# Kernel optimization log

Hardware: AMD Instinct MI355X
Metric: run time of the kernel (lower is better)

## Reference

```python
import jax, jax.numpy as jnp
import numpy as np

B, T_ENC, T_DEC = 64, 256, 200
MEL, R = 80, 2
ENC_DIM = 256   # must equal attention_context_dim (context = weighted sum of encoder outputs)
ATT = 256       # attention_rnn_units == attention_context_dim
DEC = 256       # decoder_rnn_units
PRE1, PRE2 = 256, 128


def _gru(x, h, wih, whh, bih, bhh):
    # torch.nn.GRUCell math; weights are (3*H, in) torch layout
    gi = x @ wih.T + bih
    gh = h @ whh.T + bhh
    i_r, i_z, i_n = jnp.split(gi, 3, axis=-1)
    h_r, h_z, h_n = jnp.split(gh, 3, axis=-1)
    r = jax.nn.sigmoid(i_r + h_r)
    z = jax.nn.sigmoid(i_z + h_z)
    n = jnp.tanh(i_n + r * h_n)
    return (1.0 - z) * n + z * h


def setup_inputs() -> dict:
    key = jax.random.key(0)
    ks = iter(jax.random.split(key, 40))
    def nrm(shape, s=0.05):
        return jax.random.normal(next(ks), shape, dtype=jnp.float32) * s
    inp = {
        "encoder_outputs": nrm((B, T_ENC, ENC_DIM), 1.0),
        "inputs": nrm((B, T_DEC, MEL * R), 1.0),
        "memory_lengths": jax.random.randint(next(ks), (B,), T_ENC // 2, T_ENC + 1),
        # prenet
        "pre_w1": nrm((PRE1, MEL * R)), "pre_b1": jnp.zeros((PRE1,), jnp.float32),
        "pre_w2": nrm((PRE2, PRE1)),    "pre_b2": jnp.zeros((PRE2,), jnp.float32),
        # memory layer (no bias)
        "mem_w": nrm((ATT, ENC_DIM)),
        # attention GRUCell: input = prenet_out(128) + context(256)
        "att_wih": nrm((3 * ATT, PRE2 + ATT)), "att_whh": nrm((3 * ATT, ATT)),
        "att_bih": jnp.zeros((3 * ATT,), jnp.float32), "att_bhh": jnp.zeros((3 * ATT,), jnp.float32),
        # Bahdanau attention: query layer (no bias) and v vector
        "q_w": nrm((ATT, ATT)), "v_w": nrm((ATT,)),
        # project_to_decoder_in
        "proj_w": nrm((DEC, ATT + ATT)), "proj_b": jnp.zeros((DEC,), jnp.float32),
        # two decoder GRUCells
        "g1_wih": nrm((3 * DEC, DEC)), "g1_whh": nrm((3 * DEC, DEC)),
        "g1_bih": jnp.zeros((3 * DEC,), jnp.float32), "g1_bhh": jnp.zeros((3 * DEC,), jnp.float32),
        "g2_wih": nrm((3 * DEC, DEC)), "g2_whh": nrm((3 * DEC, DEC)),
        "g2_bih": jnp.zeros((3 * DEC,), jnp.float32), "g2_bhh": jnp.zeros((3 * DEC,), jnp.float32),
        # output projections
        "mel_w": nrm((MEL * R, DEC + ATT)), "mel_b": jnp.zeros((MEL * R,), jnp.float32),
        "stop_w": nrm((1, DEC + ATT)),      "stop_b": jnp.zeros((1,), jnp.float32),
    }
    return inp


def reference(encoder_outputs, inputs, memory_lengths,
              pre_w1, pre_b1, pre_w2, pre_b2, mem_w,
              att_wih, att_whh, att_bih, att_bhh, q_w, v_w,
              proj_w, proj_b,
              g1_wih, g1_whh, g1_bih, g1_bhh,
              g2_wih, g2_whh, g2_bih, g2_bhh,
              mel_w, mel_b, stop_w, stop_b):
    b = encoder_outputs.shape[0]
    processed_memory = encoder_outputs @ mem_w.T                    # (B,T_enc,ATT)
    pad_mask = jnp.arange(T_ENC)[None, :] >= memory_lengths[:, None]  # True = padding

    # teacher forcing: step t consumes previous target frame (zeros at t=0)
    x_seq = jnp.concatenate([jnp.zeros((b, 1, MEL * R), inputs.dtype), inputs[:, :-1]], axis=1)
    xs = jnp.swapaxes(x_seq, 0, 1)                                  # (T_dec,B,mel*r)

    def step(carry, x):
        h_att, ctx, h1, h2 = carry
        # prenet (dropout omitted: deterministic reference)
        pre = jax.nn.relu(jax.nn.relu(x @ pre_w1.T + pre_b1) @ pre_w2.T + pre_b2)
        # attention RNN
        h_att = _gru(jnp.concatenate([pre, ctx], -1), h_att, att_wih, att_whh, att_bih, att_bhh)
        # Bahdanau alignment
        score = jnp.einsum('btd,d->bt', jnp.tanh(processed_memory + (h_att @ q_w.T)[:, None, :]), v_w)
        score = jnp.where(pad_mask, -jnp.inf, score)
        align = jax.nn.softmax(score, axis=-1)                      # (B,T_enc)
        ctx = jnp.einsum('bt,btd->bd', align, encoder_outputs)      # (B,ATT)
        # decoder stack with residuals
        d = jnp.concatenate([h_att, ctx], -1) @ proj_w.T + proj_b
        h1 = _gru(d, h1, g1_wih, g1_whh, g1_bih, g1_bhh); d = h1 + d
        h2 = _gru(d, h2, g2_wih, g2_whh, g2_bih, g2_bhh); d = h2 + d
        p = jnp.concatenate([d, ctx], -1)
        mel = p @ mel_w.T + mel_b                                   # (B,mel*r)
        stop = jax.nn.sigmoid(p @ stop_w.T + stop_b)[:, 0]          # (B,)
        return (h_att, ctx, h1, h2), (mel, align, stop)

    zeros = lambda d: jnp.zeros((b, d), encoder_outputs.dtype)
    init = (zeros(ATT), zeros(ATT), zeros(DEC), zeros(DEC))
    _, (mels, aligns, stops) = jax.lax.scan(step, init, xs)

    mel_outputs = jnp.swapaxes(mels, 0, 1)                          # (B,T_dec,mel*r)
    attn_scores = jnp.swapaxes(aligns, 0, 1)                        # (B,T_dec,T_enc)
    stop_tokens = jnp.repeat(jnp.swapaxes(stops, 0, 1), R, axis=1)  # (B,T_dec*r)
    return mel_outputs, attn_scores, stop_tokens
```

## Files before the change

### kernel.cpp

```cpp
#include <hip/hip_runtime.h>
#include <math.h>
#include <stdint.h>

#define NB   64
#define TE   256
#define TD   200
#define MR   160

typedef _Float16 h2 __attribute__((ext_vector_type(2)));

__device__ __forceinline__ float dot2f(h2 a, h2 b, float c){
  return __builtin_amdgcn_fdot2(a, b, c, false);
}
__device__ __forceinline__ h2 u2h(unsigned int u){ return __builtin_bit_cast(h2, u); }
__device__ __forceinline__ unsigned int h2u(h2 h){ return __builtin_bit_cast(unsigned int, h); }

__device__ __forceinline__ float sigmf(float x){
  return __fdividef(1.f, 1.f + __expf(-x));
}
__device__ __forceinline__ float tanhf_(float x){
  float ax = fabsf(x);
  float e  = __expf(-2.f*ax);
  float r  = __fdividef(1.f - e, 1.f + e);
  return copysignf(r, x);
}

static constexpr size_t OFF_PM   = 0;
static constexpr size_t OFF_ENCH = 8388608;
static constexpr size_t OFF_GIP  = 16777216;
static constexpr size_t OFF_P    = 36438016;
static constexpr size_t OFF_W2   = 49545216;
static constexpr size_t OFF_W8   = 50184192;
static constexpr size_t WS_NEEDED = 52936704;

static constexpr size_t A_PW1  = 0;
static constexpr size_t A_PW2  = 20480;
static constexpr size_t A_WIHP = 36864;
static constexpr size_t A_MEMW = 86016;
static constexpr size_t A_MELW = 118784;

static constexpr size_t B_ATTC = 0;
static constexpr size_t B_ATTH = 24576;
static constexpr size_t B_G1I  = 49152;
static constexpr size_t B_G1H  = 73728;
static constexpr size_t B_G2I  = 98304;
static constexpr size_t B_G2H  = 122880;
static constexpr size_t B_PROJ = 147456;
static constexpr size_t B_QW   = 163840;

__global__ void k_conv(const float* __restrict__ src, char* __restrict__ ws,
                       unsigned off_h2, int O, int Kh, int k0, int ld){
  int i = blockIdx.x*256 + threadIdx.x;
  if (i >= O*Kh) return;
  int o = i % O, kp = i / O;
  _Float16* dst = (_Float16*)(ws + OFF_W2) + 2*((size_t)off_h2 + i);
  dst[0] = (_Float16)src[(size_t)o*ld + k0 + 2*kp    ];
  dst[1] = (_Float16)src[(size_t)o*ld + k0 + 2*kp + 1];
}

__global__ void k_conv8(const float* __restrict__ src, char* __restrict__ ws,
                        unsigned off16, int O, int Kq, int k0, int ld){
  int i = blockIdx.x*256 + threadIdx.x;
  if (i >= O*Kq) return;
  int o = i % O, kq = i / O;
  const float* s = src + (size_t)o*ld + k0 + kq*8;
  h2 p0, p1, p2, p3;
  p0.x=(_Float16)s[0]; p0.y=(_Float16)s[1];
  p1.x=(_Float16)s[2]; p1.y=(_Float16)s[3];
  p2.x=(_Float16)s[4]; p2.y=(_Float16)s[5];
  p3.x=(_Float16)s[6]; p3.y=(_Float16)s[7];
  uint4 r; r.x=h2u(p0); r.y=h2u(p1); r.z=h2u(p2); r.w=h2u(p3);
  ((uint4*)(ws + OFF_W8))[(size_t)off16 + i] = r;
}

__global__ void k_pm(const float* __restrict__ enc, char* __restrict__ ws){
  int bt = blockIdx.x;
  int b  = bt >> 8, t = bt & 255;
  int j  = threadIdx.x;
  const h2* mw = (const h2*)(ws + OFF_W2) + A_MEMW;
  _Float16* pmT  = (_Float16*)(ws + OFF_PM);
  _Float16* encH = (_Float16*)(ws + OFF_ENCH);
  __shared__ _Float16 e[256];
  float ev = enc[(size_t)bt*256 + j];
  e[j] = (_Float16)ev;
  encH[(size_t)bt*256 + j] = (_Float16)ev;
  __syncthreads();
  const h2* e2 = (const h2*)e;
  float acc = 0.f;
  #pragma unroll 8
  for (int kp=0; kp<128; ++kp) acc = dot2f(mw[kp*256 + j], e2[kp], acc);
  pmT[(size_t)b*TE*256 + (size_t)j*TE + t] = (_Float16)acc;
}

__global__ void k_pre(const float* __restrict__ xin, const float* __restrict__ b1,
                      const float* __restrict__ b2, const float* __restrict__ bih,
                      char* __restrict__ ws){
  int bt = blockIdx.x;
  int b = bt / TD, t = bt % TD;
  int j = threadIdx.x;
  const h2* w1 = (const h2*)(ws + OFF_W2) + A_PW1;
  const h2* w2 = (const h2*)(ws + OFF_W2) + A_PW2;
  const h2* wp = (const h2*)(ws + OFF_W2) + A_WIHP;
  _Float16* gip = (_Float16*)(ws + OFF_GIP) + (size_t)bt*768;
  __shared__ _Float16 xh[160];
  __shared__ _Float16 a1[256];
  __shared__ _Float16 pr[128];
  if (j < 160)
    xh[j] = (t==0) ? (_Float16)0.f : (_Float16)xin[((size_t)b*TD + (t-1))*MR + j];
  __syncthreads();
  {
    const h2* x2 = (const h2*)xh;
    float acc = b1[j];
    #pragma unroll 8
    for (int kp=0; kp<80; ++kp) acc = dot2f(w1[kp*256 + j], x2[kp], acc);
    a1[j] = (_Float16)fmaxf(acc, 0.f);
  }
  __syncthreads();
  if (j < 128){
    const h2* x2 = (const h2*)a1;
    float acc = b2[j];
    #pragma unroll 8
    for (int kp=0; kp<128; ++kp) acc = dot2f(w2[kp*128 + j], x2[kp], acc);
    pr[j] = (_Float16)fmaxf(acc, 0.f);
  }
  __syncthreads();
  {
    const h2* p2 = (const h2*)pr;
    for (int o=j; o<768; o+=256){
      float acc = bih[o];
      #pragma unroll 8
      for (int kp=0; kp<64; ++kp) acc = dot2f(wp[kp*768 + o], p2[kp], acc);
      gip[o] = (_Float16)acc;
    }
  }
}

__global__ void k_zero(float* __restrict__ out){
  int* prog = (int*)(out + (size_t)NB*TD*MR + (size_t)NB*TD*TE);
  if (threadIdx.x < NB) prog[threadIdx.x] = 0;
}

__device__ __forceinline__ float d4dot(uint4 w, uint4 x, float a){
  a = dot2f(u2h(w.x), u2h(x.x), a);
  a = dot2f(u2h(w.y), u2h(x.y), a);
  a = dot2f(u2h(w.z), u2h(x.z), a);
  a = dot2f(u2h(w.w), u2h(x.w), a);
  return a;
}

__device__ __forceinline__ void gemv6(const uint4* __restrict__ wI, const uint4* __restrict__ wH,
                                      const uint4* xI, const uint4* xH,
                                      int j, int ks, float* scr, int tid){
  float a0=0.f,a1=0.f,a2=0.f,a3=0.f,a4=0.f,a5=0.f;
  #pragma unroll 2
  for (int kq=ks*8; kq<ks*8+8; ++kq){
    uint4 xi = xI[kq];
    uint4 xh = xH[kq];
    uint4 w0 = wI[kq*768 +       j];
    uint4 w1 = wI[kq*768 + 256 + j];
    uint4 w2 = wI[kq*768 + 512 + j];
    a0 = d4dot(w0, xi, a0);
    a1 = d4dot(w1, xi, a1);
    a2 = d4dot(w2, xi, a2);
    uint4 w3 = wH[kq*768 +       j];
    uint4 w4 = wH[kq*768 + 256 + j];
    uint4 w5 = wH[kq*768 + 512 + j];
    a3 = d4dot(w3, xh, a3);
    a4 = d4dot(w4, xh, a4);
    a5 = d4dot(w5, xh, a5);
  }
  float* r = scr + tid*6;
  r[0]=a0; r[1]=a1; r[2]=a2; r[3]=a3; r[4]=a4; r[5]=a5;
}

__global__ __launch_bounds__(1024) void k_dec(
    const int*   __restrict__ memlen,
    const float* __restrict__ att_bhh,
    const float* __restrict__ vw,
    const float* __restrict__ proj_b,
    const float* __restrict__ g1_bih, const float* __restrict__ g1_bhh,
    const float* __restrict__ g2_bih, const float* __restrict__ g2_bhh,
    float* __restrict__ out, char* __restrict__ ws)
{
  const int tid  = threadIdx.x;
  const int x    = blockIdx.x;
  const int b    = ((x >> 4) << 3) + (x & 7);
  const int role = (x >> 3) & 1;
  const int ks   = tid >> 8;
  const int j    = tid & 255;

  const uint4* W8   = (const uint4*)(ws + OFF_W8);
  const uint4* wAC  = W8 + B_ATTC;
  const uint4* wAH  = W8 + B_ATTH;
  const uint4* wG1I = W8 + B_G1I;
  const uint4* wG1H = W8 + B_G1H;
  const uint4* wG2I = W8 + B_G2I;
  const uint4* wG2H = W8 + B_G2H;
  const uint4* wPRJ = W8 + B_PROJ;
  const uint4* wQ   = W8 + B_QW;

  int* prog = (int*)(out + (size_t)NB*TD*MR + (size_t)NB*TD*TE);
  unsigned* dX = (unsigned*)((_Float16*)(ws + OFF_GIP) + (size_t)b*TD*768);

  __shared__ __align__(16) _Float16 hAh[256], ctxh[256], h1h[256], h2h[256], dh[256];
  __shared__ float hAf[256], h1f[256], h2f[256], df[256];
  __shared__ float qf[256], sc[256], al[256], vl[256];
  __shared__ float scr[6144];
  __shared__ float red2[4];

  if (role == 0){
    const _Float16* pmB  = (const _Float16*)(ws + OFF_PM)   + (size_t)b*TE*256;
    const unsigned* encW = (const unsigned*)(ws + OFF_ENCH) + (size_t)b*TE*128;
    const _Float16* gipB = (const _Float16*)(ws + OFF_GIP)  + (size_t)b*TD*768;
    _Float16*       pstB = (_Float16*)(ws + OFF_P)          + (size_t)b*TD*512;
    float* outA = out + (size_t)NB*TD*MR + (size_t)b*TD*TE;

    if (tid < 256){
      hAh[tid]=(_Float16)0.f; ctxh[tid]=(_Float16)0.f;
      hAf[tid]=0.f; vl[tid]=vw[tid];
    }
    const int ml = memlen[b];
    __syncthreads();

    const uint4* hA4  = (const uint4*)hAh;
    const uint4* ctx4 = (const uint4*)ctxh;

    #pragma unroll 1
    for (int t=0; t<TD; ++t){
      gemv6(wAC, wAH, ctx4, hA4, j, ks, scr, tid);
      __syncthreads();
      if (tid < 256){
        const _Float16* gp = gipB + (size_t)t*768;
        float s0 = scr[tid*6+0]+scr[(256+tid)*6+0]+scr[(512+tid)*6+0]+scr[(768+tid)*6+0];
        float s1 = scr[tid*6+1]+scr[(256+tid)*6+1]+scr[(512+tid)*6+1]+scr[(768+tid)*6+1];
        float s2 = scr[tid*6+2]+scr[(256+tid)*6+2]+scr[(512+tid)*6+2]+scr[(768+tid)*6+2];
        float s3 = scr[tid*6+3]+scr[(256+tid)*6+3]+scr[(512+tid)*6+3]+scr[(768+tid)*6+3];
        float s4 = scr[tid*6+4]+scr[(256+tid)*6+4]+scr[(512+tid)*6+4]+scr[(768+tid)*6+4];
        float s5 = scr[tid*6+5]+scr[(256+tid)*6+5]+scr[(512+tid)*6+5]+scr[(768+tid)*6+5];
        float gir = s0 + (float)gp[tid];
        float giz = s1 + (float)gp[256+tid];
        float gin = s2 + (float)gp[512+tid];
        float ghr = s3 + att_bhh[tid];
        float ghz = s4 + att_bhh[256+tid];
        float ghn = s5 + att_bhh[512+tid];
        float r = sigmf(gir+ghr), z = sigmf(giz+ghz);
        float n = tanhf_(gin + r*ghn);
        float h = (1.f-z)*n + z*hAf[tid];
        hAf[tid]=h; hAh[tid]=(_Float16)h;
      }
      __syncthreads();
      {
        float a=0.f;
        #pragma unroll 2
        for (int kq=ks*8; kq<ks*8+8; ++kq)
          a = d4dot(wQ[kq*256 + j], hA4[kq], a);
        scr[tid]=a;
      }
      __syncthreads();
      if (tid<256) qf[tid] = scr[tid]+scr[256+tid]+scr[512+tid]+scr[768+tid];
      __syncthreads();
      {
        const int d0 = ks*64;
        float s=0.f;
        #pragma unroll 8
        for (int d=d0; d<d0+64; ++d){
          float pv = (float)pmB[(size_t)d*TE + j];
          s += vl[d]*tanhf_(pv + qf[d]);
        }
        scr[tid]=s;
      }
      __syncthreads();
      if (tid<256){
        float s = scr[tid]+scr[256+tid]+scr[512+tid]+scr[768+tid];
        sc[tid] = (tid < ml) ? s : -INFINITY;
      }
      __syncthreads();
      {
        float v = (tid<256) ? sc[tid] : -INFINITY;
        if (tid<256){
          #pragma unroll
          for (int o=32;o>0;o>>=1) v = fmaxf(v, __shfl_down(v,o,64));
          if ((tid&63)==0) red2[tid>>6]=v;
        }
        __syncthreads();
        float m = fmaxf(fmaxf(red2[0],red2[1]), fmaxf(red2[2],red2[3]));
        __syncthreads();
        float e = 0.f;
        if (tid<256){
          e = __expf(sc[tid]-m);
          float sv = e;
          #pragma unroll
          for (int o=32;o>0;o>>=1) sv += __shfl_down(sv,o,64);
          if ((tid&63)==0) red2[tid>>6]=sv;
        }
        __syncthreads();
        if (tid<256){
          float sum = red2[0]+red2[1]+red2[2]+red2[3];
          float a = e*__fdividef(1.f,sum);
          al[tid]=a;
          outA[(size_t)t*TE + tid]=a;
        }
      }
      __syncthreads();
      {
        const int tsl = tid>>7, dp = tid&127;
        float c0=0.f, c1=0.f;
        #pragma unroll 8
        for (int tp=tsl*32; tp<tsl*32+32; ++tp){
          float a = al[tp];
          h2 e = u2h(encW[(size_t)tp*128 + dp]);
          c0 += a*(float)e.x; c1 += a*(float)e.y;
        }
        scr[tid*2]=c0; scr[tid*2+1]=c1;
      }
      __syncthreads();
      if (tid<128){
        float c0=0.f, c1=0.f;
        #pragma unroll
        for (int k=0;k<8;++k){ c0 += scr[(k*128+tid)*2]; c1 += scr[(k*128+tid)*2+1]; }
        h2 c; c.x=(_Float16)c0; c.y=(_Float16)c1;
        unsigned w = h2u(c);
        ((unsigned*)ctxh)[tid] = w;
        ((unsigned*)pstB)[(size_t)t*256 + 128 + tid] = w;
      }
      __syncthreads();
      {
        const uint4* xa = (ks<2) ? hA4 : ctx4;
        const int    kb = (ks<2) ? 0 : 32;
        float a=0.f;
        #pragma unroll 2
        for (int kq=ks*16; kq<ks*16+16; ++kq)
          a = d4dot(wPRJ[kq*256 + j], xa[kq-kb], a);
        scr[tid]=a;
      }
      __syncthreads();
      if (tid<128){
        const int o0 = 2*tid, o1 = o0+1;
        float dv0 = scr[o0]+scr[256+o0]+scr[512+o0]+scr[768+o0] + proj_b[o0];
        float dv1 = scr[o1]+scr[256+o1]+scr[512+o1]+scr[768+o1] + proj_b[o1];
        h2 p; p.x=(_Float16)dv0; p.y=(_Float16)dv1;
        __hip_atomic_store(dX + (size_t)t*384 + tid, h2u(p),
                           __ATOMIC_RELAXED, __HIP_MEMORY_SCOPE_AGENT);
      }
      __syncthreads();
      if (tid==0)
        __hip_atomic_store(&prog[b], t+1,
                           __ATOMIC_RELEASE, __HIP_MEMORY_SCOPE_AGENT);
    }
  } else {
    _Float16* pstB = (_Float16*)(ws + OFF_P) + (size_t)b*TD*512;

    if (tid < 256){
      h1h[tid]=(_Float16)0.f; h2h[tid]=(_Float16)0.f;
      h1f[tid]=0.f; h2f[tid]=0.f;
    }
    __syncthreads();

    const uint4* h14 = (const uint4*)h1h;
    const uint4* h24 = (const uint4*)h2h;
    const uint4* dd4 = (const uint4*)dh;

    #pragma unroll 1
    for (int t=0; t<TD; ++t){
      if (tid==0){
        while (__hip_atomic_load(&prog[b], __ATOMIC_RELAXED, __HIP_MEMORY_SCOPE_AGENT) < t+1)
          __builtin_amdgcn_s_sleep(1);
      }
      __syncthreads();
      if (tid<128){
        unsigned w = __hip_atomic_load(dX + (size_t)t*384 + tid,
                                       __ATOMIC_RELAXED, __HIP_MEMORY_SCOPE_AGENT);
        ((unsigned*)dh)[tid] = w;
        h2 p = u2h(w);
        df[2*tid]   = (float)p.x;
        df[2*tid+1] = (float)p.y;
      }
      __syncthreads();
      gemv6(wG1I, wG1H, dd4, h14, j, ks, scr, tid);
      __syncthreads();
      if (tid<256){
        float s0 = scr[tid*6+0]+scr[(256+tid)*6+0]+scr[(512+tid)*6+0]+scr[(768+tid)*6+0];
        float s1 = scr[tid*6+1]+scr[(256+tid)*6+1]+scr[(512+tid)*6+1]+scr[(768+tid)*6+1];
        float s2 = scr[tid*6+2]+scr[(256+tid)*6+2]+scr[(512+tid)*6+2]+scr[(768+tid)*6+2];
        float s3 = scr[tid*6+3]+scr[(256+tid)*6+3]+scr[(512+tid)*6+3]+scr[(768+tid)*6+3];
        float s4 = scr[tid*6+4]+scr[(256+tid)*6+4]+scr[(512+tid)*6+4]+scr[(768+tid)*6+4];
        float s5 = scr[tid*6+5]+scr[(256+tid)*6+5]+scr[(512+tid)*6+5]+scr[(768+tid)*6+5];
        float gir = s0 + g1_bih[tid];
        float giz = s1 + g1_bih[256+tid];
        float gin = s2 + g1_bih[512+tid];
        float ghr = s3 + g1_bhh[tid];
        float ghz = s4 + g1_bhh[256+tid];
        float ghn = s5 + g1_bhh[512+tid];
        float r = sigmf(gir+ghr), z = sigmf(giz+ghz);
        float n = tanhf_(gin + r*ghn);
        float h = (1.f-z)*n + z*h1f[tid];
        float dn = h + df[tid];
        h1f[tid]=h; h1h[tid]=(_Float16)h;
        df[tid]=dn; dh[tid]=(_Float16)dn;
      }
      __syncthreads();
      gemv6(wG2I, wG2H, dd4, h24, j, ks, scr, tid);
      __syncthreads();
      if (tid<256){
        float s0 = scr[tid*6+0]+scr[(256+tid)*6+0]+scr[(512+tid)*6+0]+scr[(768+tid)*6+0];
        float s1 = scr[tid*6+1]+scr[(256+tid)*6+1]+scr[(512+tid)*6+1]+scr[(768+tid)*6+1];
        float s2 = scr[tid*6+2]+scr[(256+tid)*6+2]+scr[(512+tid)*6+2]+scr[(768+tid)*6+2];
        float s3 = scr[tid*6+3]+scr[(256+tid)*6+3]+scr[(512+tid)*6+3]+scr[(768+tid)*6+3];
        float s4 = scr[tid*6+4]+scr[(256+tid)*6+4]+scr[(512+tid)*6+4]+scr[(768+tid)*6+4];
        float s5 = scr[tid*6+5]+scr[(256+tid)*6+5]+scr[(512+tid)*6+5]+scr[(768+tid)*6+5];
        float gir = s0 + g2_bih[tid];
        float giz = s1 + g2_bih[256+tid];
        float gin = s2 + g2_bih[512+tid];
        float ghr = s3 + g2_bhh[tid];
        float ghz = s4 + g2_bhh[256+tid];
        float ghn = s5 + g2_bhh[512+tid];
        float r = sigmf(gir+ghr), z = sigmf(giz+ghz);
        float n = tanhf_(gin + r*ghn);
        float h = (1.f-z)*n + z*h2f[tid];
        float dn = h + df[tid];
        h2f[tid]=h; h2h[tid]=(_Float16)h;
        pstB[(size_t)t*512 + tid] = (_Float16)dn;
      }
      __syncthreads();
    }
  }
}

__global__ void k_post(const float* __restrict__ mel_b, const float* __restrict__ stop_w,
                       const float* __restrict__ stop_b, float* __restrict__ out,
                       char* __restrict__ ws){
  int bt = blockIdx.x;
  int b = bt / TD, t = bt % TD;
  int j = threadIdx.x;
  const h2* wm = (const h2*)(ws + OFF_W2) + A_MELW;
  const _Float16* p = (const _Float16*)(ws + OFF_P) + (size_t)bt*512;
  __shared__ _Float16 pl[512];
  ((uint32_t*)pl)[j] = ((const uint32_t*)p)[j];
  __syncthreads();
  const h2* p2 = (const h2*)pl;
  if (j < 160){
    float acc = mel_b[j];
    #pragma unroll 8
    for (int kp=0; kp<256; ++kp) acc = dot2f(wm[kp*160 + j], p2[kp], acc);
    out[(size_t)bt*MR + j] = acc;
  } else if (j == 160){
    float acc = stop_b[0];
    for (int k=0; k<512; ++k) acc += stop_w[k]*(float)pl[k];
    float s = __fdividef(1.f, 1.f + __expf(-acc));
    float* os = out + (size_t)NB*TD*MR + (size_t)NB*TD*TE + (size_t)b*2*TD;
    os[2*t]   = s;
    os[2*t+1] = s;
  }
}

extern "C" void kernel_launch(void* const* d_in, const int* in_sizes, int n_in,
                              void* d_out, int out_size, void* d_ws, size_t ws_size,
                              hipStream_t stream)
{
  const float* enc     = (const float*)d_in[0];
  const float* xin     = (const float*)d_in[1];
  const int*   mlen    = (const int*)  d_in[2];
  const float* pre_w1  = (const float*)d_in[3];
  const float* pre_b1  = (const float*)d_in[4];
  const float* pre_w2  = (const float*)d_in[5];
  const float* pre_b2  = (const float*)d_in[6];
  const float* mem_w   = (const float*)d_in[7];
  const float* att_wih = (const float*)d_in[8];
  const float* att_whh = (const float*)d_in[9];
  const float* att_bih = (const float*)d_in[10];
  const float* att_bhh = (const float*)d_in[11];
  const float* q_w     = (const float*)d_in[12];
  const float* v_w     = (const float*)d_in[13];
  const float* proj_w  = (const float*)d_in[14];
  const float* proj_b  = (const float*)d_in[15];
  const float* g1_wih  = (const float*)d_in[16];
  const float* g1_whh  = (const float*)d_in[17];
  const float* g1_bih  = (const float*)d_in[18];
  const float* g1_bhh  = (const float*)d_in[19];
  const float* g2_wih  = (const float*)d_in[20];
  const float* g2_whh  = (const float*)d_in[21];
  const float* g2_bih  = (const float*)d_in[22];
  const float* g2_bhh  = (const float*)d_in[23];
  const float* mel_w   = (const float*)d_in[24];
  const float* mel_b   = (const float*)d_in[25];
  const float* stop_w  = (const float*)d_in[26];
  const float* stop_b  = (const float*)d_in[27];
  (void)in_sizes; (void)n_in; (void)out_size;

  if (ws_size < WS_NEEDED) return;

  float* out = (float*)d_out;
  char*  ws  = (char*)d_ws;

  auto conv = [&](const float* src, size_t off_h2, int O, int Kh, int k0, int ld){
    int n = O*Kh;
    k_conv<<<(n+255)/256, 256, 0, stream>>>(src, ws, (unsigned)off_h2, O, Kh, k0, ld);
  };
  auto conv8 = [&](const float* src, size_t off16, int O, int Kq, int k0, int ld){
    int n = O*Kq;
    k_conv8<<<(n+255)/256, 256, 0, stream>>>(src, ws, (unsigned)off16, O, Kq, k0, ld);
  };

  conv(pre_w1,  A_PW1,  256, 80,  0, 160);
  conv(pre_w2,  A_PW2,  128, 128, 0, 256);
  conv(att_wih, A_WIHP, 768, 64,  0, 384);
  conv(mem_w,   A_MEMW, 256, 128, 0, 256);
  conv(mel_w,   A_MELW, 160, 256, 0, 512);
  conv8(att_wih, B_ATTC, 768, 32, 128, 384);
  conv8(att_whh, B_ATTH, 768, 32, 0,   256);
  conv8(g1_wih,  B_G1I,  768, 32, 0,   256);
  conv8(g1_whh,  B_G1H,  768, 32, 0,   256);
  conv8(g2_wih,  B_G2I,  768, 32, 0,   256);
  conv8(g2_whh,  B_G2H,  768, 32, 0,   256);
  conv8(proj_w,  B_PROJ, 256, 64, 0,   512);
  conv8(q_w,     B_QW,   256, 32, 0,   256);

  k_pm  <<<NB*TE, 256, 0, stream>>>(enc, ws);
  k_pre <<<NB*TD, 256, 0, stream>>>(xin, pre_b1, pre_b2, att_bih, ws);
  k_zero<<<1, 64, 0, stream>>>(out);
  k_dec <<<2*NB, 1024, 0, stream>>>(mlen, att_bhh, v_w, proj_b,
                                    g1_bih, g1_bhh, g2_bih, g2_bhh, out, ws);
  k_post<<<NB*TD, 256, 0, stream>>>(mel_b, stop_w, stop_b, out, ws);
}
```

Measured before the change: 5.497 ms.

## Split decoder into four pipelined roles per batch with flag-based handoff

The recurrent decoder moves from two 1024-thread blocks per batch element to four 512-thread blocks: attention GRU, attention+projection, decoder GRU1, and decoder GRU2, linked through global progress flags and staged fp16 vectors. The aim is to pipeline the stages across timesteps so that GRU1/GRU2 and the attention GRU overlap instead of running serially. It also precomputes the hidden-state half of each GRU before waiting, and keeps the query weights, processed memory (now row-major) and encoder values in registers inside the attention role. In exchange it adds cross-block spin-wait latency on every step, uses more blocks, and increases register pressure. It also reuses the start of the output buffer as scratch space for GRU1 outputs.

```diff
diff --git a/kernel.cpp b/kernel.cpp
--- a/kernel.cpp
+++ b/kernel.cpp
@@ -75,10 +75,9 @@
 
 __global__ void k_pm(const float* __restrict__ enc, char* __restrict__ ws){
   int bt = blockIdx.x;
-  int b  = bt >> 8, t = bt & 255;
   int j  = threadIdx.x;
   const h2* mw = (const h2*)(ws + OFF_W2) + A_MEMW;
-  _Float16* pmT  = (_Float16*)(ws + OFF_PM);
+  _Float16* pmN  = (_Float16*)(ws + OFF_PM);
   _Float16* encH = (_Float16*)(ws + OFF_ENCH);
   __shared__ _Float16 e[256];
   float ev = enc[(size_t)bt*256 + j];
@@ -89,7 +88,7 @@
   float acc = 0.f;
   #pragma unroll 8
   for (int kp=0; kp<128; ++kp) acc = dot2f(mw[kp*256 + j], e2[kp], acc);
-  pmT[(size_t)b*TE*256 + (size_t)j*TE + t] = (_Float16)acc;
+  pmN[(size_t)bt*256 + j] = (_Float16)acc;
 }
 
 __global__ void k_pre(const float* __restrict__ xin, const float* __restrict__ b1,
@@ -137,7 +136,7 @@
 
 __global__ void k_zero(float* __restrict__ out){
   int* prog = (int*)(out + (size_t)NB*TD*MR + (size_t)NB*TD*TE);
-  if (threadIdx.x < NB) prog[threadIdx.x] = 0;
+  if (threadIdx.x < 256) prog[threadIdx.x] = 0;
 }
 
 __device__ __forceinline__ float d4dot(uint4 w, uint4 x, float a){
@@ -148,32 +147,23 @@
   return a;
 }
 
-__device__ __forceinline__ void gemv6(const uint4* __restrict__ wI, const uint4* __restrict__ wH,
-                                      const uint4* xI, const uint4* xH,
-                                      int j, int ks, float* scr, int tid){
-  float a0=0.f,a1=0.f,a2=0.f,a3=0.f,a4=0.f,a5=0.f;
-  #pragma unroll 2
-  for (int kq=ks*8; kq<ks*8+8; ++kq){
-    uint4 xi = xI[kq];
-    uint4 xh = xH[kq];
-    uint4 w0 = wI[kq*768 +       j];
-    uint4 w1 = wI[kq*768 + 256 + j];
-    uint4 w2 = wI[kq*768 + 512 + j];
-    a0 = d4dot(w0, xi, a0);
-    a1 = d4dot(w1, xi, a1);
-    a2 = d4dot(w2, xi, a2);
-    uint4 w3 = wH[kq*768 +       j];
-    uint4 w4 = wH[kq*768 + 256 + j];
-    uint4 w5 = wH[kq*768 + 512 + j];
-    a3 = d4dot(w3, xh, a3);
-    a4 = d4dot(w4, xh, a4);
-    a5 = d4dot(w5, xh, a5);
+__device__ __forceinline__ void gemv3(const uint4* __restrict__ w, const uint4* x,
+                                      int j, int ks, float& r0, float& r1, float& r2){
+  float a0=0.f, a1=0.f, a2=0.f;
+  #pragma unroll 4
+  for (int kq=ks*16; kq<ks*16+16; ++kq){
+    uint4 xv = x[kq];
+    uint4 w0 = w[kq*768 +       j];
+    uint4 w1 = w[kq*768 + 256 + j];
+    uint4 w2 = w[kq*768 + 512 + j];
+    a0 = d4dot(w0, xv, a0);
+    a1 = d4dot(w1, xv, a1);
+    a2 = d4dot(w2, xv, a2);
   }
-  float* r = scr + tid*6;
-  r[0]=a0; r[1]=a1; r[2]=a2; r[3]=a3; r[4]=a4; r[5]=a5;
-}
-
-__global__ __launch_bounds__(1024) void k_dec(
+  r0=a0; r1=a1; r2=a2;
+}
+
+__global__ __launch_bounds__(512,1) void k_dec(
     const int*   __restrict__ memlen,
     const float* __restrict__ att_bhh,
     const float* __restrict__ vw,
@@ -184,59 +174,59 @@
 {
   const int tid  = threadIdx.x;
   const int x    = blockIdx.x;
-  const int b    = ((x >> 4) << 3) + (x & 7);
-  const int role = (x >> 3) & 1;
+  const int y    = x >> 3;
+  const int role = y & 3;
+  const int b    = ((y >> 2) << 3) | (x & 7);
   const int ks   = tid >> 8;
   const int j    = tid & 255;
 
-  const uint4* W8   = (const uint4*)(ws + OFF_W8);
-  const uint4* wAC  = W8 + B_ATTC;
-  const uint4* wAH  = W8 + B_ATTH;
-  const uint4* wG1I = W8 + B_G1I;
-  const uint4* wG1H = W8 + B_G1H;
-  const uint4* wG2I = W8 + B_G2I;
-  const uint4* wG2H = W8 + B_G2H;
-  const uint4* wPRJ = W8 + B_PROJ;
-  const uint4* wQ   = W8 + B_QW;
-
+  const uint4* W8 = (const uint4*)(ws + OFF_W8);
   int* prog = (int*)(out + (size_t)NB*TD*MR + (size_t)NB*TD*TE);
-  unsigned* dX = (unsigned*)((_Float16*)(ws + OFF_GIP) + (size_t)b*TD*768);
-
-  __shared__ __align__(16) _Float16 hAh[256], ctxh[256], h1h[256], h2h[256], dh[256];
-  __shared__ float hAf[256], h1f[256], h2f[256], df[256];
+  int* pA1  = prog;
+  int* pCtx = prog + 64;
+  int* pD   = prog + 128;
+  int* pB1  = prog + 192;
+  unsigned* gX = (unsigned*)((_Float16*)(ws + OFF_GIP) + (size_t)b*TD*768);
+
+  __shared__ __align__(16) _Float16 hAh[256], ctxh[256], hh[256], dh[256];
+  __shared__ float hAf[256], hf[256], df[256];
   __shared__ float qf[256], sc[256], al[256], vl[256];
-  __shared__ float scr[6144];
+  __shared__ float scr[3072];
   __shared__ float red2[4];
 
   if (role == 0){
-    const _Float16* pmB  = (const _Float16*)(ws + OFF_PM)   + (size_t)b*TE*256;
-    const unsigned* encW = (const unsigned*)(ws + OFF_ENCH) + (size_t)b*TE*128;
-    const _Float16* gipB = (const _Float16*)(ws + OFF_GIP)  + (size_t)b*TD*768;
-    _Float16*       pstB = (_Float16*)(ws + OFF_P)          + (size_t)b*TD*512;
-    float* outA = out + (size_t)NB*TD*MR + (size_t)b*TD*TE;
-
-    if (tid < 256){
-      hAh[tid]=(_Float16)0.f; ctxh[tid]=(_Float16)0.f;
-      hAf[tid]=0.f; vl[tid]=vw[tid];
-    }
-    const int ml = memlen[b];
+    const uint4* wAC = W8 + B_ATTC;
+    const uint4* wAH = W8 + B_ATTH;
+    const _Float16* gipB = (const _Float16*)(ws + OFF_GIP) + (size_t)b*TD*768;
+    if (tid < 256){ hAh[tid]=(_Float16)0.f; hAf[tid]=0.f; ctxh[tid]=(_Float16)0.f; }
     __syncthreads();
-
     const uint4* hA4  = (const uint4*)hAh;
     const uint4* ctx4 = (const uint4*)ctxh;
-
     #pragma unroll 1
     for (int t=0; t<TD; ++t){
-      gemv6(wAC, wAH, ctx4, hA4, j, ks, scr, tid);
+      float a3,a4,a5; gemv3(wAH, hA4, j, ks, a3,a4,a5);
+      if (t > 0){
+        if (tid==0){
+          while (__hip_atomic_load(pCtx+b, __ATOMIC_RELAXED, __HIP_MEMORY_SCOPE_AGENT) < t)
+            __builtin_amdgcn_s_sleep(1);
+        }
+        __syncthreads();
+        if (tid<128)
+          ((unsigned*)ctxh)[tid] = __hip_atomic_load(gX + (size_t)(t-1)*384 + 128 + tid,
+                                                     __ATOMIC_RELAXED, __HIP_MEMORY_SCOPE_AGENT);
+        __syncthreads();
+      }
+      float a0,a1,a2; gemv3(wAC, ctx4, j, ks, a0,a1,a2);
+      { float* r = scr + tid*6; r[0]=a0;r[1]=a1;r[2]=a2;r[3]=a3;r[4]=a4;r[5]=a5; }
       __syncthreads();
       if (tid < 256){
         const _Float16* gp = gipB + (size_t)t*768;
-        float s0 = scr[tid*6+0]+scr[(256+tid)*6+0]+scr[(512+tid)*6+0]+scr[(768+tid)*6+0];
-        float s1 = scr[tid*6+1]+scr[(256+tid)*6+1]+scr[(512+tid)*6+1]+scr[(768+tid)*6+1];
-        float s2 = scr[tid*6+2]+scr[(256+tid)*6+2]+scr[(512+tid)*6+2]+scr[(768+tid)*6+2];
-        float s3 = scr[tid*6+3]+scr[(256+tid)*6+3]+scr[(512+tid)*6+3]+scr[(768+tid)*6+3];
-        float s4 = scr[tid*6+4]+scr[(256+tid)*6+4]+scr[(512+tid)*6+4]+scr[(768+tid)*6+4];
-        float s5 = scr[tid*6+5]+scr[(256+tid)*6+5]+scr[(512+tid)*6+5]+scr[(768+tid)*6+5];
+        float s0 = scr[tid*6+0]+scr[(256+tid)*6+0];
+        float s1 = scr[tid*6+1]+scr[(256+tid)*6+1];
+        float s2 = scr[tid*6+2]+scr[(256+tid)*6+2];
+        float s3 = scr[tid*6+3]+scr[(256+tid)*6+3];
+        float s4 = scr[tid*6+4]+scr[(256+tid)*6+4];
+        float s5 = scr[tid*6+5]+scr[(256+tid)*6+5];
         float gir = s0 + (float)gp[tid];
         float giz = s1 + (float)gp[256+tid];
         float gin = s2 + (float)gp[512+tid];
@@ -249,29 +239,72 @@
         hAf[tid]=h; hAh[tid]=(_Float16)h;
       }
       __syncthreads();
-      {
-        float a=0.f;
-        #pragma unroll 2
-        for (int kq=ks*8; kq<ks*8+8; ++kq)
-          a = d4dot(wQ[kq*256 + j], hA4[kq], a);
-        scr[tid]=a;
-      }
-      __syncthreads();
-      if (tid<256) qf[tid] = scr[tid]+scr[256+tid]+scr[512+tid]+scr[768+tid];
-      __syncthreads();
-      {
-        const int d0 = ks*64;
-        float s=0.f;
-        #pragma unroll 8
-        for (int d=d0; d<d0+64; ++d){
-          float pv = (float)pmB[(size_t)d*TE + j];
-          s += vl[d]*tanhf_(pv + qf[d]);
-        }
-        scr[tid]=s;
-      }
+      if (tid<128)
+        __hip_atomic_store(gX + (size_t)t*384 + tid, ((const unsigned*)hAh)[tid],
+                           __ATOMIC_RELAXED, __HIP_MEMORY_SCOPE_AGENT);
+      __syncthreads();
+      if (tid==0)
+        __hip_atomic_store(pA1+b, t+1, __ATOMIC_RELEASE, __HIP_MEMORY_SCOPE_AGENT);
+    }
+  } else if (role == 1){
+    const uint4* wPRJ = W8 + B_PROJ;
+    const uint4* wQ4  = W8 + B_QW;
+    const uint4* pm4  = (const uint4*)(ws + OFF_PM) + (size_t)b*8192;
+    const unsigned* encW = (const unsigned*)(ws + OFF_ENCH) + (size_t)b*TE*128;
+    _Float16* pstB = (_Float16*)(ws + OFF_P) + (size_t)b*TD*512;
+    float* outA = out + (size_t)NB*TD*MR + (size_t)b*TD*TE;
+    const int ml = memlen[b];
+    const int tsl = tid>>7, dp = tid&127;
+
+    uint4 wq[16], pmr[16];
+    unsigned er[64];
+    #pragma unroll
+    for (int i=0;i<16;++i) wq[i]  = wQ4[(ks*16+i)*256 + j];
+    #pragma unroll
+    for (int i=0;i<16;++i) pmr[i] = pm4[(size_t)j*32 + ks*16 + i];
+    #pragma unroll
+    for (int i=0;i<64;++i) er[i]  = encW[(size_t)(tsl*64+i)*128 + dp];
+    if (tid<256) vl[tid] = vw[tid];
+    __syncthreads();
+    const uint4* hA4  = (const uint4*)hAh;
+    const uint4* ctx4 = (const uint4*)ctxh;
+
+    #pragma unroll 1
+    for (int t=0; t<TD; ++t){
+      if (tid==0){
+        while (__hip_atomic_load(pA1+b, __ATOMIC_RELAXED, __HIP_MEMORY_SCOPE_AGENT) < t+1)
+          __builtin_amdgcn_s_sleep(1);
+      }
+      __syncthreads();
+      if (tid<128)
+        ((unsigned*)hAh)[tid] = __hip_atomic_load(gX + (size_t)t*384 + tid,
+                                                  __ATOMIC_RELAXED, __HIP_MEMORY_SCOPE_AGENT);
+      __syncthreads();
+      { float a=0.f;
+        #pragma unroll
+        for (int i=0;i<16;++i) a = d4dot(wq[i], hA4[ks*16+i], a);
+        scr[tid]=a; }
+      __syncthreads();
+      if (tid<256) qf[tid] = scr[tid]+scr[256+tid];
+      __syncthreads();
+      { float s=0.f;
+        #pragma unroll
+        for (int i=0;i<16;++i){
+          uint4 q4 = pmr[i]; int d0 = ks*128 + i*8;
+          h2 p0=u2h(q4.x), p1=u2h(q4.y), p2=u2h(q4.z), p3=u2h(q4.w);
+          s += vl[d0+0]*tanhf_((float)p0.x + qf[d0+0]);
+          s += vl[d0+1]*tanhf_((float)p0.y + qf[d0+1]);
+          s += vl[d0+2]*tanhf_((float)p1.x + qf[d0+2]);
+          s += vl[d0+3]*tanhf_((float)p1.y + qf[d0+3]);
+          s += vl[d0+4]*tanhf_((float)p2.x + qf[d0+4]);
+          s += vl[d0+5]*tanhf_((float)p2.y + qf[d0+5]);
+          s += vl[d0+6]*tanhf_((float)p3.x + qf[d0+6]);
+          s += vl[d0+7]*tanhf_((float)p3.y + qf[d0+7]);
+        }
+        scr[tid]=s; }
       __syncthreads();
       if (tid<256){
-        float s = scr[tid]+scr[256+tid]+scr[512+tid]+scr[768+tid];
+        float s = scr[tid]+scr[256+tid];
         sc[tid] = (tid < ml) ? s : -INFINITY;
       }
       __syncthreads();
@@ -302,73 +335,76 @@
         }
       }
       __syncthreads();
-      {
-        const int tsl = tid>>7, dp = tid&127;
-        float c0=0.f, c1=0.f;
-        #pragma unroll 8
-        for (int tp=tsl*32; tp<tsl*32+32; ++tp){
-          float a = al[tp];
-          h2 e = u2h(encW[(size_t)tp*128 + dp]);
+      { float c0=0.f, c1=0.f;
+        #pragma unroll
+        for (int i=0;i<64;++i){
+          float a = al[tsl*64+i];
+          h2 e = u2h(er[i]);
           c0 += a*(float)e.x; c1 += a*(float)e.y;
         }
-        scr[tid*2]=c0; scr[tid*2+1]=c1;
-      }
+        scr[tid*2]=c0; scr[tid*2+1]=c1; }
       __syncthreads();
       if (tid<128){
         float c0=0.f, c1=0.f;
         #pragma unroll
-        for (int k=0;k<8;++k){ c0 += scr[(k*128+tid)*2]; c1 += scr[(k*128+tid)*2+1]; }
+        for (int k=0;k<4;++k){ c0 += scr[(k*128+tid)*2]; c1 += scr[(k*128+tid)*2+1]; }
         h2 c; c.x=(_Float16)c0; c.y=(_Float16)c1;
         unsigned w = h2u(c);
         ((unsigned*)ctxh)[tid] = w;
         ((unsigned*)pstB)[(size_t)t*256 + 128 + tid] = w;
-      }
-      __syncthreads();
-      {
-        const uint4* xa = (ks<2) ? hA4 : ctx4;
-        const int    kb = (ks<2) ? 0 : 32;
-        float a=0.f;
-        #pragma unroll 2
-        for (int kq=ks*16; kq<ks*16+16; ++kq)
-          a = d4dot(wPRJ[kq*256 + j], xa[kq-kb], a);
-        scr[tid]=a;
-      }
+        __hip_atomic_store(gX + (size_t)t*384 + 128 + tid, w,
+                           __ATOMIC_RELAXED, __HIP_MEMORY_SCOPE_AGENT);
+      }
+      __syncthreads();
+      if (tid==0)
+        __hip_atomic_store(pCtx+b, t+1, __ATOMIC_RELEASE, __HIP_MEMORY_SCOPE_AGENT);
+      { float a=0.f;
+        #pragma unroll 4
+        for (int kq=ks*32; kq<ks*32+32; ++kq){
+          uint4 xa = (ks==0) ? hA4[kq] : ctx4[kq-32];
+          a = d4dot(wPRJ[kq*256 + j], xa, a);
+        }
+        scr[tid]=a; }
       __syncthreads();
       if (tid<128){
         const int o0 = 2*tid, o1 = o0+1;
-        float dv0 = scr[o0]+scr[256+o0]+scr[512+o0]+scr[768+o0] + proj_b[o0];
-        float dv1 = scr[o1]+scr[256+o1]+scr[512+o1]+scr[768+o1] + proj_b[o1];
-        h2 p; p.x=(_Float16)dv0; p.y=(_Float16)dv1;
-        __hip_atomic_store(dX + (size_t)t*384 + tid, h2u(p),
+        float d0 = scr[o0]+scr[256+o0] + proj_b[o0];
+        float d1 = scr[o1]+scr[256+o1] + proj_b[o1];
+        h2 p; p.x=(_Float16)d0; p.y=(_Float16)d1;
+        __hip_atomic_store(gX + (size_t)t*384 + 256 + tid, h2u(p),
                            __ATOMIC_RELAXED, __HIP_MEMORY_SCOPE_AGENT);
       }
       __syncthreads();
       if (tid==0)
-        __hip_atomic_store(&prog[b], t+1,
-                           __ATOMIC_RELEASE, __HIP_MEMORY_SCOPE_AGENT);
+        __hip_atomic_store(pD+b, t+1, __ATOMIC_RELEASE, __HIP_MEMORY_SCOPE_AGENT);
     }
   } else {
+    const bool isB1 = (role == 2);
+    const uint4* wI = W8 + (isB1 ? B_G1I : B_G2I);
+    const uint4* wH = W8 + (isB1 ? B_G1H : B_G2H);
+    const float* bih = isB1 ? g1_bih : g2_bih;
+    const float* bhh = isB1 ? g1_bhh : g2_bhh;
+    int* pin = isB1 ? pD : pB1;
+    unsigned* oX = (unsigned*)out + (size_t)b*TD*128;
+    const unsigned* inP = isB1 ? (gX + 256) : oX;
+    const int instr = isB1 ? 384 : 128;
     _Float16* pstB = (_Float16*)(ws + OFF_P) + (size_t)b*TD*512;
 
-    if (tid < 256){
-      h1h[tid]=(_Float16)0.f; h2h[tid]=(_Float16)0.f;
-      h1f[tid]=0.f; h2f[tid]=0.f;
-    }
+    if (tid<256){ hh[tid]=(_Float16)0.f; hf[tid]=0.f; }
     __syncthreads();
-
-    const uint4* h14 = (const uint4*)h1h;
-    const uint4* h24 = (const uint4*)h2h;
+    const uint4* h4  = (const uint4*)hh;
     const uint4* dd4 = (const uint4*)dh;
 
     #pragma unroll 1
     for (int t=0; t<TD; ++t){
+      float a3,a4,a5; gemv3(wH, h4, j, ks, a3,a4,a5);
       if (tid==0){
-        while (__hip_atomic_load(&prog[b], __ATOMIC_RELAXED, __HIP_MEMORY_SCOPE_AGENT) < t+1)
+        while (__hip_atomic_load(pin+b, __ATOMIC_RELAXED, __HIP_MEMORY_SCOPE_AGENT) < t+1)
           __builtin_amdgcn_s_sleep(1);
       }
       __syncthreads();
       if (tid<128){
-        unsigned w = __hip_atomic_load(dX + (size_t)t*384 + tid,
+        unsigned w = __hip_atomic_load(inP + (size_t)t*instr + tid,
                                        __ATOMIC_RELAXED, __HIP_MEMORY_SCOPE_AGENT);
         ((unsigned*)dh)[tid] = w;
         h2 p = u2h(w);
@@ -376,52 +412,39 @@
         df[2*tid+1] = (float)p.y;
       }
       __syncthreads();
-      gemv6(wG1I, wG1H, dd4, h14, j, ks, scr, tid);
+      float a0,a1,a2; gemv3(wI, dd4, j, ks, a0,a1,a2);
+      { float* r = scr + tid*6; r[0]=a0;r[1]=a1;r[2]=a2;r[3]=a3;r[4]=a4;r[5]=a5; }
       __syncthreads();
       if (tid<256){
-        float s0 = scr[tid*6+0]+scr[(256+tid)*6+0]+scr[(512+tid)*6+0]+scr[(768+tid)*6+0];
-        float s1 = scr[tid*6+1]+scr[(256+tid)*6+1]+scr[(512+tid)*6+1]+scr[(768+tid)*6+1];
-        float s2 = scr[tid*6+2]+scr[(256+tid)*6+2]+scr[(512+tid)*6+2]+scr[(768+tid)*6+2];
-        float s3 = scr[tid*6+3]+scr[(256+tid)*6+3]+scr[(512+tid)*6+3]+scr[(768+tid)*6+3];
-        float s4 = scr[tid*6+4]+scr[(256+tid)*6+4]+scr[(512+tid)*6+4]+scr[(768+tid)*6+4];
-        float s5 = scr[tid*6+5]+scr[(256+tid)*6+5]+scr[(512+tid)*6+5]+scr[(768+tid)*6+5];
-        float gir = s0 + g1_bih[tid];
-        float giz = s1 + g1_bih[256+tid];
-        float gin = s2 + g1_bih[512+tid];
-        float ghr = s3 + g1_bhh[tid];
-        float ghz = s4 + g1_bhh[256+tid];
-        float ghn = s5 + g1_bhh[512+tid];
+        float s0 = scr[tid*6+0]+scr[(256+tid)*6+0];
+        float s1 = scr[tid*6+1]+scr[(256+tid)*6+1];
+        float s2 = scr[tid*6+2]+scr[(256+tid)*6+2];
+        float s3 = scr[tid*6+3]+scr[(256+tid)*6+3];
+        float s4 = scr[tid*6+4]+scr[(256+tid)*6+4];
+        float s5 = scr[tid*6+5]+scr[(256+tid)*6+5];
+        float gir = s0 + bih[tid];
+        float giz = s1 + bih[256+tid];
+        float gin = s2 + bih[512+tid];
+        float ghr = s3 + bhh[tid];
+        float ghz = s4 + bhh[256+tid];
+        float ghn = s5 + bhh[512+tid];
         float r = sigmf(gir+ghr), z = sigmf(giz+ghz);
         float n = tanhf_(gin + r*ghn);
-        float h = (1.f-z)*n + z*h1f[tid];
+        float h = (1.f-z)*n + z*hf[tid];
         float dn = h + df[tid];
-        h1f[tid]=h; h1h[tid]=(_Float16)h;
-        df[tid]=dn; dh[tid]=(_Float16)dn;
-      }
-      __syncthreads();
-      gemv6(wG2I, wG2H, dd4, h24, j, ks, scr, tid);
-      __syncthreads();
-      if (tid<256){
-        float s0 = scr[tid*6+0]+scr[(256+tid)*6+0]+scr[(512+tid)*6+0]+scr[(768+tid)*6+0];
-        float s1 = scr[tid*6+1]+scr[(256+tid)*6+1]+scr[(512+tid)*6+1]+scr[(768+tid)*6+1];
-        float s2 = scr[tid*6+2]+scr[(256+tid)*6+2]+scr[(512+tid)*6+2]+scr[(768+tid)*6+2];
-        float s3 = scr[tid*6+3]+scr[(256+tid)*6+3]+scr[(512+tid)*6+3]+scr[(768+tid)*6+3];
-        float s4 = scr[tid*6+4]+scr[(256+tid)*6+4]+scr[(512+tid)*6+4]+scr[(768+tid)*6+4];
-        float s5 = scr[tid*6+5]+scr[(256+tid)*6+5]+scr[(512+tid)*6+5]+scr[(768+tid)*6+5];
-        float gir = s0 + g2_bih[tid];
-        float giz = s1 + g2_bih[256+tid];
-        float gin = s2 + g2_bih[512+tid];
-        float ghr = s3 + g2_bhh[tid];
-        float ghz = s4 + g2_bhh[256+tid];
-        float ghn = s5 + g2_bhh[512+tid];
-        float r = sigmf(gir+ghr), z = sigmf(giz+ghz);
-        float n = tanhf_(gin + r*ghn);
-        float h = (1.f-z)*n + z*h2f[tid];
-        float dn = h + df[tid];
-        h2f[tid]=h; h2h[tid]=(_Float16)h;
-        pstB[(size_t)t*512 + tid] = (_Float16)dn;
-      }
-      __syncthreads();
+        hf[tid]=h; hh[tid]=(_Float16)h;
+        dh[tid]=(_Float16)dn;
+        if (!isB1) pstB[(size_t)t*512 + tid] = (_Float16)dn;
+      }
+      __syncthreads();
+      if (isB1){
+        if (tid<128)
+          __hip_atomic_store(oX + (size_t)t*128 + tid, ((const unsigned*)dh)[tid],
+                             __ATOMIC_RELAXED, __HIP_MEMORY_SCOPE_AGENT);
+        __syncthreads();
+        if (tid==0)
+          __hip_atomic_store(pB1+b, t+1, __ATOMIC_RELEASE, __HIP_MEMORY_SCOPE_AGENT);
+      }
     }
   }
 }
@@ -517,8 +540,8 @@
 
   k_pm  <<<NB*TE, 256, 0, stream>>>(enc, ws);
   k_pre <<<NB*TD, 256, 0, stream>>>(xin, pre_b1, pre_b2, att_bih, ws);
-  k_zero<<<1, 64, 0, stream>>>(out);
-  k_dec <<<2*NB, 1024, 0, stream>>>(mlen, att_bhh, v_w, proj_b,
-                                    g1_bih, g1_bhh, g2_bih, g2_bhh, out, ws);
+  k_zero<<<1, 256, 0, stream>>>(out);
+  k_dec <<<4*NB, 512, 0, stream>>>(mlen, att_bhh, v_w, proj_b,
+                                   g1_bih, g1_bhh, g2_bih, g2_bhh, out, ws);
   k_post<<<NB*TD, 256, 0, stream>>>(mel_b, stop_w, stop_b, out, ws);
 }
```

New measurement: 10.94 ms. +99.0%, slower.
